# Optimization experiments

Measured on AMD Instinct MI355X. Metric: run time of the kernel, lower is better.

## Reference

```python
import jax, jax.numpy as jnp
from jax import lax
import numpy as np

WINDOW = 7
SIGMA = 1.5
DATA_RANGE = 2.0
SSIM_WEIGHT = 0.5
VQ_WEIGHT = 1.0
FG_WEIGHT = 5.0
BG_THRESHOLD = -0.9


def _gaussian_1d(dtype=jnp.float32):
    coords = jnp.arange(WINDOW, dtype=dtype) - (WINDOW - 1) / 2.0
    g = jnp.exp(-coords ** 2 / (2.0 * SIGMA ** 2))
    return g / g.sum()


def _blur3d(x, g):
    # Separable gaussian blur == dense 7x7x7 gaussian conv (kernel is an outer product).
    # x: (B,1,D,H,W); three 1D passes along D, H, W with SAME (zero) padding.
    dn = ('NCDHW', 'OIDHW', 'NCDHW')
    for shape in [(1, 1, WINDOW, 1, 1), (1, 1, 1, WINDOW, 1), (1, 1, 1, 1, WINDOW)]:
        x = lax.conv_general_dilated(x, g.reshape(shape), (1, 1, 1), 'SAME',
                                     dimension_numbers=dn)
    return x


def ssim3d(x, y):
    C1 = (0.01 * DATA_RANGE) ** 2
    C2 = (0.03 * DATA_RANGE) ** 2
    g = _gaussian_1d(x.dtype)
    mu_x = _blur3d(x, g)
    mu_y = _blur3d(y, g)
    mu_x2, mu_y2, mu_xy = mu_x * mu_x, mu_y * mu_y, mu_x * mu_y
    sigma_x2 = _blur3d(x * x, g) - mu_x2
    sigma_y2 = _blur3d(y * y, g) - mu_y2
    sigma_xy = _blur3d(x * y, g) - mu_xy
    ssim_map = (2 * mu_xy + C1) * (2 * sigma_xy + C2) / (
        (mu_x2 + mu_y2 + C1) * (sigma_x2 + sigma_y2 + C2))
    return ssim_map.mean()


def weighted_l1(recon, target):
    w = jnp.where(target > BG_THRESHOLD, FG_WEIGHT, 1.0).astype(recon.dtype)
    return jnp.sum(w * jnp.abs(recon - target)) / jnp.sum(w)


def setup_inputs() -> dict:
    key = jax.random.key(0)
    k1, k2, k3 = jax.random.split(key, 3)
    shape = (4, 1, 160, 192, 192)
    recon = jax.random.normal(k1, shape, dtype=jnp.float32)
    target = jax.random.normal(k2, shape, dtype=jnp.float32)
    vq_loss = jax.random.uniform(k3, (), dtype=jnp.float32)
    return {"recon": recon, "target": target, "vq_loss": vq_loss}


def reference(recon, target, vq_loss):
    l1 = weighted_l1(recon, target)
    ssim_term = 1.0 - ssim3d(recon.astype(jnp.float32), target.astype(jnp.float32))
    rec = l1 + SSIM_WEIGHT * ssim_term
    total = rec + VQ_WEIGHT * vq_loss
    return total
```

## Files before the change

kernel.cpp:

```cpp
#include <hip/hip_runtime.h>
#include <math.h>

typedef __attribute__((ext_vector_type(2))) float f32x2;
typedef __attribute__((ext_vector_type(4))) float f32x4;

#define BDIM 4
#define DDIM 160
#define HDIM 192
#define WDIM 192
#define NTOT (BDIM * DDIM * HDIM * WDIM)
#define SLICEPX (HDIM * WDIM)

template<int N> struct IC { static constexpr int v = N; };

__device__ __forceinline__ float rcp_fast(float x) {
#if __has_builtin(__builtin_amdgcn_rcpf)
    return __builtin_amdgcn_rcpf(x);
#else
    return 1.0f / x;
#endif
}

__device__ __forceinline__ unsigned cvtpk(float lo, float hi) {
    unsigned r;
    asm("v_cvt_pk_bf16_f32 %0, %1, %2" : "=v"(r) : "v"(lo), "v"(hi));
    return r;
}

#define G7INIT { 0.03663285f, 0.11128076f, 0.21674532f, 0.27068215f, \
                 0.21674532f, 0.11128076f, 0.03663285f }

#define STEP_BARRIER() do {                                   \
    asm volatile("s_waitcnt lgkmcnt(0)" ::: "memory");        \
    __builtin_amdgcn_s_barrier();                             \
} while (0)

#define ATH 8
#define ARH 14
#define HBW 200
#define NSL 166
#define SPB 4
#define NTH 512

struct PFBuf { f32x4 x0, y0, x1, y1; };

__global__ __launch_bounds__(NTH, 4)
void nq_fields(const float* __restrict__ X, const float* __restrict__ Y,
               uint2* __restrict__ F, float2* __restrict__ pl1)
{
    constexpr float Gc[7] = G7INIT;
    __shared__ __align__(16) f32x2 raw[2][ARH][WDIM];
    __shared__ __align__(16) f32x2 hA[2][ATH][HBW];
    __shared__ __align__(16) f32x2 hB[2][ATH][HBW];
    __shared__ float red[NTH / 64][2];
    ;

    const int t = threadIdx.x;
    const int strip = blockIdx.x;
    const int z = blockIdx.z;
    const int h0 = strip * ATH;
    const int b0 = blockIdx.y * SPB;

    const int r0 = t / 48, c0 = (t % 48) * 4;
    const int h0r0 = h0 + r0 - 3;
    const bool okh0 = (unsigned)h0r0 < (unsigned)HDIM;
    const bool int0 = (r0 >= 3) && (r0 < 11);
    const int off0 = h0r0 * WDIM + c0;
    const int lof0 = r0 * WDIM + c0;

    const bool act1 = t < 160;
    const int i4b = 512 + t;
    const int r1 = i4b / 48, c1 = (i4b % 48) * 4;
    const int h0r1 = h0 + r1 - 3;
    const bool okh1 = act1 && ((unsigned)h0r1 < (unsigned)HDIM);
    const bool int1 = act1 && (r1 >= 3) && (r1 < 11);
    const int off1 = h0r1 * WDIM + c1;
    const int lof1 = r1 * WDIM + c1;

    const int hr0 = t / 96,         hw0 = (t % 96) * 2;
    const int hr1 = (t + 512) / 96, hw1 = ((t + 512) % 96) * 2;
    const bool hact1 = t < 256;

    const int wr0 = t / 96,         ww0 = (t % 96) * 2;
    const int wr1 = (t + 512) / 96, ww1 = ((t + 512) % 96) * 2;

    if (t < 128) {
        const int pp = t >> 6, r = (t >> 3) & 7, c8 = t & 7;
        const int col = (c8 < 4) ? c8 : (192 + c8);
        hA[pp][r][col] = (f32x2){0.f, 0.f};
        hB[pp][r][col] = (f32x2){0.f, 0.f};
    }

    float l1n = 0.f, l1d = 0.f;
    PFBuf pfA, pfB;

    auto validby = [&](int by) { return (by >= 3) && (by < 163); };

    auto issue = [&](PFBuf& p, int by) {
        const int d = by - 3;
        const size_t sbase = ((size_t)z * DDIM + d) * SLICEPX;
        const f32x4 zz = {0.f, 0.f, 0.f, 0.f};
        p.x0 = okh0 ? *(const f32x4*)(X + sbase + off0) : zz;
        p.y0 = okh0 ? *(const f32x4*)(Y + sbase + off0) : zz;
        p.x1 = okh1 ? *(const f32x4*)(X + sbase + off1) : zz;
        p.y1 = okh1 ? *(const f32x4*)(Y + sbase + off1) : zz;
    };

    __shared__ __align__(16) f32x2 rawbuf[ARH][WDIM];

    auto commit = [&](PFBuf& p) {
        if (int0) {
            #pragma unroll
            for (int j = 0; j < 4; ++j) {
                const float x = p.x0[j], y = p.y0[j];
                const float wgt = (y > -0.9f) ? 5.f : 1.f;
                l1n += wgt * fabsf(x - y);
                l1d += wgt;
            }
        }
        if (int1) {
            #pragma unroll
            for (int j = 0; j < 4; ++j) {
                const float x = p.x1[j], y = p.y1[j];
                const float wgt = (y > -0.9f) ? 5.f : 1.f;
                l1n += wgt * fabsf(x - y);
                l1d += wgt;
            }
        }
        f32x2* r = &rawbuf[0][0];
        *(f32x4*)(r + lof0)     = (f32x4){p.x0.x + p.y0.x, p.x0.x - p.y0.x,
                                          p.x0.y + p.y0.y, p.x0.y - p.y0.y};
        *(f32x4*)(r + lof0 + 2) = (f32x4){p.x0.z + p.y0.z, p.x0.z - p.y0.z,
                                          p.x0.w + p.y0.w, p.x0.w - p.y0.w};
        if (act1) {
            *(f32x4*)(r + lof1)     = (f32x4){p.x1.x + p.y1.x, p.x1.x - p.y1.x,
                                              p.x1.y + p.y1.y, p.x1.y - p.y1.y};
            *(f32x4*)(r + lof1 + 2) = (f32x4){p.x1.z + p.y1.z, p.x1.z - p.y1.z,
                                              p.x1.w + p.y1.w, p.x1.w - p.y1.w};
        }
    };

    auto hitem = [&](int hp, int r, int w0) {
        f32x2 aA0 = {0.f, 0.f}, aA1 = {0.f, 0.f};
        f32x2 aB0 = {0.f, 0.f}, aB1 = {0.f, 0.f};
        #pragma unroll
        for (int k = 0; k < 7; ++k) {
            const f32x4 v = *(const f32x4*)(&rawbuf[r + k][w0]);
            const f32x2 p0 = {v.x, v.y}, p1 = {v.z, v.w};
            const float g = Gc[k];
            aA0 += g * p0; aB0 += (g * p0) * p0;
            aA1 += g * p1; aB1 += (g * p1) * p1;
        }
        *(f32x4*)(&hA[hp][r][4 + w0]) = (f32x4){aA0.x, aA0.y, aA1.x, aA1.y};
        *(f32x4*)(&hB[hp][r][4 + w0]) = (f32x4){aB0.x, aB0.y, aB1.x, aB1.y};
    };

    auto witem = [&](int hp, int r, int w0, size_t obase) {
        f32x2 vA[10], vB[10];
        #pragma unroll
        for (int j = 0; j < 5; ++j) {
            const f32x4 qa = *(const f32x4*)(&hA[hp][r][w0 + 2 * j]);
            vA[2 * j] = (f32x2){qa.x, qa.y}; vA[2 * j + 1] = (f32x2){qa.z, qa.w};
            const f32x4 qb = *(const f32x4*)(&hB[hp][r][w0 + 2 * j]);
            vB[2 * j] = (f32x2){qb.x, qb.y}; vB[2 * j + 1] = (f32x2){qb.z, qb.w};
        }
        f32x2 a0 = {0.f, 0.f}, a1 = {0.f, 0.f};
        f32x2 e0 = {0.f, 0.f}, e1 = {0.f, 0.f};
        #pragma unroll
        for (int k = 0; k < 7; ++k) {
            const float g = Gc[k];
            a0 += g * vA[1 + k]; a1 += g * vA[2 + k];
            e0 += g * vB[1 + k]; e1 += g * vB[2 + k];
        }
        uint4 o;
        o.x = cvtpk(a0.x, a0.y);
        o.y = cvtpk(e0.x, e0.y);
        o.z = cvtpk(a1.x, a1.y);
        o.w = cvtpk(e1.x, e1.y);
        *(uint4*)&F[obase + (size_t)(h0 + r) * WDIM + w0] = o;
    };

    auto wstore = [&](int hp, int by) {
        const size_t obase = ((size_t)z * NSL + by) * SLICEPX;
        witem(hp, wr0, ww0, obase);
        if (hact1) witem(hp, wr1, ww1, obase);
    };

    if (validby(b0))     { issue(pfB, b0); commit(pfB); }
    if (validby(b0 + 1)) issue(pfB, b0 + 1);
    STEP_BARRIER();

    auto iter = [&](auto ICi) {
        constexpr int i = ICi.v;
        const int c = b0 + i;
        PFBuf& ld = (i % 2 == 0) ? pfA : pfB;
        PFBuf& cm = (i % 2 == 0) ? pfB : pfA;
        if (i < 2 && validby(c + 2)) issue(ld, c + 2);
        if (validby(c)) {
            hitem(i & 1, hr0, hw0);
            if (hact1) hitem(i & 1, hr1, hw1);
        }
        STEP_BARRIER();
        if (i >= 1 && validby(c - 1)) wstore((i - 1) & 1, c - 1);
        if (i < 3 && validby(c + 1)) commit(cm);
        STEP_BARRIER();
    };
    iter(IC<0>{}); iter(IC<1>{}); iter(IC<2>{}); iter(IC<3>{});

    if (validby(b0 + 3)) wstore(1, b0 + 3);

    #pragma unroll
    for (int off = 32; off > 0; off >>= 1) {
        l1n += __shfl_down(l1n, off, 64);
        l1d += __shfl_down(l1d, off, 64);
    }
    const int wave = t >> 6, lane = t & 63;
    if (lane == 0) { red[wave][0] = l1n; red[wave][1] = l1d; }
    __syncthreads();
    if (t == 0) {
        float n = 0.f, dn = 0.f;
        #pragma unroll
        for (int i2 = 0; i2 < NTH / 64; ++i2) { n += red[i2][0]; dn += red[i2][1]; }
        const int bidx = (z * gridDim.y + blockIdx.y) * gridDim.x + blockIdx.x;
        pl1[bidx] = (float2){n, dn};
    }
}

__global__ __launch_bounds__(512, 4)
void nq_ssim(const uint2* __restrict__ F, float* __restrict__ pssim)
{
    constexpr float Gc[7] = G7INIT;
    constexpr float C1f = 4.0e-4f;
    constexpr float C2f = 3.6e-3f;
    __shared__ float red[8];

    const int t = threadIdx.x;
    const int p = blockIdx.x * 512 + t;
    const int gd0 = blockIdx.y * 20;
    const size_t fb = (size_t)blockIdx.z * NSL * SLICEPX;

    float ssum = 0.f;
    f32x2 wM[7], wE[7];

    auto loadF = [&](int ds) -> uint2 {
        const int di = gd0 - 3 + ds;
        if ((unsigned)di < (unsigned)DDIM)
            return F[fb + (size_t)(di + 3) * SLICEPX + p];
        return (uint2){0u, 0u};
    };

    uint2 nf = loadF(0);

    auto step = [&](auto PPc, int it) {
        constexpr int PP = PPc.v;
        const int ds = it * 7 + PP;
        if (ds < 26) {
            const uint2 cur = nf;
            if (ds + 1 < 26) nf = loadF(ds + 1);
            wM[PP] = (f32x2){__uint_as_float(cur.x << 16),
                             __uint_as_float(cur.x & 0xffff0000u)};
            wE[PP] = (f32x2){__uint_as_float(cur.y << 16),
                             __uint_as_float(cur.y & 0xffff0000u)};
            if (ds >= 6) {
                f32x2 mu = {0.f, 0.f}, e2 = {0.f, 0.f};
                #pragma unroll
                for (int k = 0; k < 7; ++k) {
                    const int s = (PP + 1 + k) % 7;
                    const float g = Gc[k];
                    mu += g * wM[s]; e2 += g * wE[s];
                }
                const float P = mu.x * mu.x, Q = mu.y * mu.y;
                const float u_ = 0.5f * (P + Q);
                const float v_ = 0.5f * (P - Q);
                const float a2 = 0.5f * (e2.x + e2.y);
                const float b2 = 0.5f * (e2.x - e2.y);
                const float num = (v_ + C1f) * (b2 - v_ + C2f);
                const float den = (u_ + C1f) * (a2 - u_ + C2f);
                ssum += num * rcp_fast(den);
            }
        }
    };

    for (int it = 0; it < 4; ++it) {
        step(IC<0>{}, it); step(IC<1>{}, it); step(IC<2>{}, it);
        step(IC<3>{}, it); step(IC<4>{}, it); step(IC<5>{}, it);
        step(IC<6>{}, it);
    }

    #pragma unroll
    for (int off = 32; off > 0; off >>= 1) ssum += __shfl_down(ssum, off, 64);
    const int wave = t >> 6, lane = t & 63;
    if (lane == 0) red[wave] = ssum;
    __syncthreads();
    if (t == 0) {
        float s = 0.f;
        #pragma unroll
        for (int i = 0; i < 8; ++i) s += red[i];
        pssim[(blockIdx.z * gridDim.y + blockIdx.y) * gridDim.x + blockIdx.x] = s;
    }
}

__global__ void nq_reduce(const float* __restrict__ pssim, int nss,
                          const float2* __restrict__ pl1, int nl1,
                          const float* __restrict__ vq, float* __restrict__ out)
{
    __shared__ float red[4][3];
    const int t = threadIdx.x;
    float s = 0.f, n = 0.f, dn = 0.f;
    for (int i = t; i < nss; i += 256) s += pssim[i];
    for (int i = t; i < nl1; i += 256) { const float2 v = pl1[i]; n += v.x; dn += v.y; }
    #pragma unroll
    for (int off = 32; off > 0; off >>= 1) {
        s  += __shfl_down(s,  off, 64);
        n  += __shfl_down(n,  off, 64);
        dn += __shfl_down(dn, off, 64);
    }
    const int wave = t >> 6, lane = t & 63;
    if (lane == 0) { red[wave][0] = s; red[wave][1] = n; red[wave][2] = dn; }
    __syncthreads();
    if (t == 0) {
        float S = 0.f, N = 0.f, DN = 0.f;
        #pragma unroll
        for (int i = 0; i < 4; ++i) { S += red[i][0]; N += red[i][1]; DN += red[i][2]; }
        out[0] = N / DN + 0.5f * (1.0f - S / (float)NTOT) + vq[0];
    }
}

#define FTH 8
#define FTW 64
#define FSEG 20
#define FNSEG (DDIM / FSEG)
#define FNS  (FSEG + 6)
#define FNTH 512
#define FRHH (FTH + 6)
#define FRWW 70
#define FNRAW (FRHH * FRWW)
#define FHBSTR 72

__global__ __launch_bounds__(FNTH, 4)
void nq_mono(const float* __restrict__ X, const float* __restrict__ Y,
             float* __restrict__ acc)
{
    constexpr float Gc[7] = G7INIT;
    constexpr float C1f = 4.0e-4f;
    constexpr float C2f = 3.6e-3f;

    __shared__ __align__(16) f32x2 raw[2][FNRAW];
    __shared__ __align__(16) f32x2 hbA[2][FTH][FHBSTR];
    __shared__ __align__(16) f32x2 hbB[2][FTH][FHBSTR];
    __shared__ float red[FNTH / 64][3];

    const int wt  = blockIdx.x;
    const int ht  = blockIdx.y;
    const int b   = blockIdx.z >> 3;
    const int seg = blockIdx.z & 7;
    const int h0 = ht * FTH, w0 = wt * FTW;
    const int dbase = seg * FSEG;
    const long long bbase = (long long)b * (DDIM * HDIM * WDIM);
    const int t = threadIdx.x;

    int goff[2]; bool ok[2], inter[2];
    #pragma unroll
    for (int i = 0; i < 2; ++i) {
        const int idx = t + i * FNTH;
        const int hh = idx / FRWW, ww = idx - hh * FRWW;
        const int h = h0 + hh - 3, w = w0 + ww - 3;
        bool o_ = ((unsigned)h < HDIM) && ((unsigned)w < WDIM);
        bool in_ = ((unsigned)(hh - 3) < FTH) && ((unsigned)(ww - 3) < FTW);
        if (i == 1 && idx >= FNRAW) { o_ = false; in_ = false; }
        ok[i] = o_; inter[i] = in_;
        goff[i] = h * WDIM + w;
    }
    const bool has1 = (t + FNTH) < FNRAW;

    const int q0r = t / FRWW,          q0w = t - q0r * FRWW;
    const int q1r = (t + FNTH) / FRWW, q1w = (t + FNTH) - q1r * FRWW;
    const bool q1on = t < (FTH * FRWW - FNTH);

    const int p4r = t >> 6;
    const int p4c = t & 63;

    float ssum = 0.f, l1n = 0.f, l1d = 0.f;
    f32x2 wA[7], wB[7];
    float pfs[2], pfd[2];

    auto loadslice = [&](int s) {
        const int d_g = dbase - 3 + s;
        const bool dok = (unsigned)d_g < (unsigned)DDIM;
        const long long sb = bbase + (long long)d_g * (HDIM * WDIM);
        const bool l1on = (s >= 3) && (s <= FSEG + 2);
        #pragma unroll
        for (int i = 0; i < 2; ++i) {
            const bool l = dok && ok[i];
            const float xv = l ? X[sb + goff[i]] : 0.f;
            const float yv = l ? Y[sb + goff[i]] : 0.f;
            if (l1on && inter[i]) {
                const float wgt = (yv > -0.9f) ? 5.f : 1.f;
                l1n += wgt * fabsf(xv - yv);
                l1d += wgt;
            }
            pfs[i] = xv + yv;
            pfd[i] = xv - yv;
        }
    };

    auto commit = [&](int s) {
        const int rb = s & 1;
        raw[rb][t] = (f32x2){pfs[0], pfd[0]};
        if (has1) raw[rb][t + FNTH] = (f32x2){pfs[1], pfd[1]};
    };

    auto p2item = [&](int rb, int r, int w) {
        f32x2 aA = {0.f, 0.f}, aB = {0.f, 0.f};
        #pragma unroll
        for (int k = 0; k < 7; ++k) {
            const f32x2 p = raw[rb][(r + k) * FRWW + w];
            const float g = Gc[k];
            aA += g * p;
            aB += (g * p) * p;
        }
        hbA[rb][r][w] = aA;
        hbB[rb][r][w] = aB;
    };

    auto phase = [&](auto PPc, int it) {
        constexpr int PP = PPc.v;
        constexpr int SLOT = (PP + 6) % 7;
        const int ps = it * 7 + PP;
        const int par = ps & 1;

        if (ps <= FNS - 2) commit(ps + 1);
        if (ps <= FNS - 3) loadslice(ps + 2);

        if (ps <= FNS - 1) {
            p2item(par, q0r, q0w);
            if (q1on) p2item(par, q1r, q1w);
        }
        if (ps >= 1 && ps <= FNS) {
            const int hp = par ^ 1;
            f32x2 a = {0.f, 0.f}, bv = {0.f, 0.f};
            #pragma unroll
            for (int k = 0; k < 7; ++k) {
                const float g = Gc[k];
                a  += g * hbA[hp][p4r][p4c + k];
                bv += g * hbB[hp][p4r][p4c + k];
            }
            wA[SLOT] = a; wB[SLOT] = bv;
            if (ps >= 7) {
                f32x2 mu = {0.f, 0.f}, e2 = {0.f, 0.f};
                #pragma unroll
                for (int k = 0; k < 7; ++k) {
                    const int s = (PP + k) % 7;
                    const float g = Gc[k];
                    mu += g * wA[s]; e2 += g * wB[s];
                }
                const float P = mu.x * mu.x, Q = mu.y * mu.y;
                const float u  = 0.5f * (P + Q);
                const float v_ = 0.5f * (P - Q);
                const float a2 = 0.5f * (e2.x + e2.y);
                const float b2 = 0.5f * (e2.x - e2.y);
                const float num = (v_ + C1f) * (b2 - v_ + C2f);
                const float den = (u  + C1f) * (a2 - u  + C2f);
                ssum += num * rcp_fast(den);
            }
        }
        __syncthreads();
    };

    loadslice(0);
    commit(0);
    loadslice(1);
    __syncthreads();

    for (int it = 0; it < 4; ++it) {
        phase(IC<0>{}, it); phase(IC<1>{}, it); phase(IC<2>{}, it);
        phase(IC<3>{}, it); phase(IC<4>{}, it); phase(IC<5>{}, it);
        phase(IC<6>{}, it);
    }

    #pragma unroll
    for (int off = 32; off > 0; off >>= 1) {
        ssum += __shfl_down(ssum, off, 64);
        l1n  += __shfl_down(l1n,  off, 64);
        l1d  += __shfl_down(l1d,  off, 64);
    }
    const int wave = t >> 6, lane = t & 63;
    if (lane == 0) { red[wave][0] = ssum; red[wave][1] = l1n; red[wave][2] = l1d; }
    __syncthreads();
    if (t == 0) {
        float s = 0.f, n = 0.f, dn = 0.f;
        #pragma unroll
        for (int i = 0; i < FNTH / 64; ++i) {
            s += red[i][0]; n += red[i][1]; dn += red[i][2];
        }
        atomicAdd(&acc[0], s);
        atomicAdd(&acc[1], n);
        atomicAdd(&acc[2], dn);
    }
}

__global__ void nq_final_acc(const float* __restrict__ acc,
                             const float* __restrict__ vq,
                             float* __restrict__ out)
{
    const float ssim_mean = acc[0] / (float)NTOT;
    out[0] = acc[1] / acc[2] + 0.5f * (1.0f - ssim_mean) + vq[0];
}

extern "C" void kernel_launch(void* const* d_in, const int* in_sizes, int n_in,
                              void* d_out, int out_size, void* d_ws, size_t ws_size,
                              hipStream_t stream)
{
    const float* X  = (const float*)d_in[0];
    const float* Y  = (const float*)d_in[1];
    const float* vq = (const float*)d_in[2];
    float* out = (float*)d_out;

    const size_t needFull = 256 + (size_t)BDIM * NSL * SLICEPX * 8;

    if (ws_size >= needFull) {
        uint2* F = (uint2*)((char*)d_ws + 256);
        char* tail = (char*)d_ws + 256 + (size_t)(3 * NSL + 163) * SLICEPX * 8;
        float*  pssim = (float*)tail;
        float2* pl1   = (float2*)(tail + 16384);

        nq_fields<<<dim3(24, 42, 4), NTH, 0, stream>>>(X, Y, F, pl1);
        nq_ssim  <<<dim3(72, 8, 4),  512, 0, stream>>>(F, pssim);
        nq_reduce<<<1, 256, 0, stream>>>(pssim, 2304, pl1, 4032, vq, out);
    } else {
        float* acc = (float*)d_ws;
        hipMemsetAsync(acc, 0, 16, stream);
        nq_mono<<<dim3(WDIM / FTW, HDIM / FTH, BDIM * FNSEG), FNTH, 0, stream>>>(X, Y, acc);
        nq_final_acc<<<1, 1, 0, stream>>>(acc, vq, out);
    }
}
```

Baseline: 134.6 us.

## Double-buffer raw slice in LDS as packed bf16 and drop a barrier

```diff
diff --git a/kernel.cpp b/kernel.cpp
--- a/kernel.cpp
+++ b/kernel.cpp
@@ -27,6 +27,10 @@
     return r;
 }
 
+__device__ __forceinline__ f32x2 unpk(unsigned u) {
+    return (f32x2){__uint_as_float(u << 16), __uint_as_float(u & 0xffff0000u)};
+}
+
 #define G7INIT { 0.03663285f, 0.11128076f, 0.21674532f, 0.27068215f, \
                  0.21674532f, 0.11128076f, 0.03663285f }
 
@@ -49,11 +53,10 @@
                uint2* __restrict__ F, float2* __restrict__ pl1)
 {
     constexpr float Gc[7] = G7INIT;
-    __shared__ __align__(16) f32x2 raw[2][ARH][WDIM];
+    __shared__ __align__(16) unsigned rawB[2][ARH][WDIM];
     __shared__ __align__(16) f32x2 hA[2][ATH][HBW];
     __shared__ __align__(16) f32x2 hB[2][ATH][HBW];
     __shared__ float red[NTH / 64][2];
-    ;
 
     const int t = threadIdx.x;
     const int strip = blockIdx.x;
@@ -92,7 +95,7 @@
     }
 
     float l1n = 0.f, l1d = 0.f;
-    PFBuf pfA, pfB;
+    PFBuf pf0, pf1;
 
     auto validby = [&](int by) { return (by >= 3) && (by < 163); };
 
@@ -106,9 +109,7 @@
         p.y1 = okh1 ? *(const f32x4*)(Y + sbase + off1) : zz;
     };
 
-    __shared__ __align__(16) f32x2 rawbuf[ARH][WDIM];
-
-    auto commit = [&](PFBuf& p) {
+    auto commit = [&](PFBuf& p, int par) {
         if (int0) {
             #pragma unroll
             for (int j = 0; j < 4; ++j) {
@@ -127,32 +128,38 @@
                 l1d += wgt;
             }
         }
-        f32x2* r = &rawbuf[0][0];
-        *(f32x4*)(r + lof0)     = (f32x4){p.x0.x + p.y0.x, p.x0.x - p.y0.x,
-                                          p.x0.y + p.y0.y, p.x0.y - p.y0.y};
-        *(f32x4*)(r + lof0 + 2) = (f32x4){p.x0.z + p.y0.z, p.x0.z - p.y0.z,
-                                          p.x0.w + p.y0.w, p.x0.w - p.y0.w};
+        {
+            uint4 u;
+            u.x = cvtpk(p.x0.x + p.y0.x, p.x0.x - p.y0.x);
+            u.y = cvtpk(p.x0.y + p.y0.y, p.x0.y - p.y0.y);
+            u.z = cvtpk(p.x0.z + p.y0.z, p.x0.z - p.y0.z);
+            u.w = cvtpk(p.x0.w + p.y0.w, p.x0.w - p.y0.w);
+            *(uint4*)(&rawB[par][0][0] + lof0) = u;
+        }
         if (act1) {
-            *(f32x4*)(r + lof1)     = (f32x4){p.x1.x + p.y1.x, p.x1.x - p.y1.x,
-                                              p.x1.y + p.y1.y, p.x1.y - p.y1.y};
-            *(f32x4*)(r + lof1 + 2) = (f32x4){p.x1.z + p.y1.z, p.x1.z - p.y1.z,
-                                              p.x1.w + p.y1.w, p.x1.w - p.y1.w};
-        }
-    };
-
-    auto hitem = [&](int hp, int r, int w0) {
+            uint4 u;
+            u.x = cvtpk(p.x1.x + p.y1.x, p.x1.x - p.y1.x);
+            u.y = cvtpk(p.x1.y + p.y1.y, p.x1.y - p.y1.y);
+            u.z = cvtpk(p.x1.z + p.y1.z, p.x1.z - p.y1.z);
+            u.w = cvtpk(p.x1.w + p.y1.w, p.x1.w - p.y1.w);
+            *(uint4*)(&rawB[par][0][0] + lof1) = u;
+        }
+    };
+
+    auto hitem = [&](int par, int r, int w0) {
         f32x2 aA0 = {0.f, 0.f}, aA1 = {0.f, 0.f};
         f32x2 aB0 = {0.f, 0.f}, aB1 = {0.f, 0.f};
         #pragma unroll
         for (int k = 0; k < 7; ++k) {
-            const f32x4 v = *(const f32x4*)(&rawbuf[r + k][w0]);
-            const f32x2 p0 = {v.x, v.y}, p1 = {v.z, v.w};
+            const uint2 u = *(const uint2*)(&rawB[par][r + k][w0]);
+            const f32x2 p0 = unpk(u.x);
+            const f32x2 p1 = unpk(u.y);
             const float g = Gc[k];
             aA0 += g * p0; aB0 += (g * p0) * p0;
             aA1 += g * p1; aB1 += (g * p1) * p1;
         }
-        *(f32x4*)(&hA[hp][r][4 + w0]) = (f32x4){aA0.x, aA0.y, aA1.x, aA1.y};
-        *(f32x4*)(&hB[hp][r][4 + w0]) = (f32x4){aB0.x, aB0.y, aB1.x, aB1.y};
+        *(f32x4*)(&hA[par][r][4 + w0]) = (f32x4){aA0.x, aA0.y, aA1.x, aA1.y};
+        *(f32x4*)(&hB[par][r][4 + w0]) = (f32x4){aB0.x, aB0.y, aB1.x, aB1.y};
     };
 
     auto witem = [&](int hp, int r, int w0, size_t obase) {
@@ -186,23 +193,20 @@
         if (hact1) witem(hp, wr1, ww1, obase);
     };
 
-    if (validby(b0))     { issue(pfB, b0); commit(pfB); }
-    if (validby(b0 + 1)) issue(pfB, b0 + 1);
+    if (validby(b0))     { issue(pf0, b0); commit(pf0, 0); }
+    if (validby(b0 + 1)) issue(pf1, b0 + 1);
     STEP_BARRIER();
 
     auto iter = [&](auto ICi) {
         constexpr int i = ICi.v;
         const int c = b0 + i;
-        PFBuf& ld = (i % 2 == 0) ? pfA : pfB;
-        PFBuf& cm = (i % 2 == 0) ? pfB : pfA;
-        if (i < 2 && validby(c + 2)) issue(ld, c + 2);
+        if (i < 2 && validby(c + 2)) issue((i == 0) ? pf0 : pf1, c + 2);
         if (validby(c)) {
             hitem(i & 1, hr0, hw0);
             if (hact1) hitem(i & 1, hr1, hw1);
         }
-        STEP_BARRIER();
-        if (i >= 1 && validby(c - 1)) wstore((i - 1) & 1, c - 1);
-        if (i < 3 && validby(c + 1)) commit(cm);
+        if (i >= 1 && validby(c - 1)) wstore((i + 1) & 1, c - 1);
+        if (i < 3 && validby(c + 1)) commit((i % 2 == 0) ? pf1 : pf0, (i + 1) & 1);
         STEP_BARRIER();
     };
     iter(IC<0>{}); iter(IC<1>{}); iter(IC<2>{}); iter(IC<3>{});
```

After: 132.7 us, median of 2. About the same (-1.4%).
